# Kernel tuning notes

Hardware: AMD Instinct MI355X
Metric: run time of the kernel (lower is better)

## Reference

```python
import jax, jax.numpy as jnp
import numpy as np

H, N_EMB, D_EMB, D_UP = 1024, 8192, 512, 2048
B, T, BB, M, K_LABELS = 4, 4096, 512, 4096, 64


def _rms(x, w, eps=1e-6):
    xf = x.astype(jnp.float32)
    var = jnp.mean(xf * xf, axis=-1, keepdims=True)
    return (w * (xf * jax.lax.rsqrt(var + eps))).astype(x.dtype)


def setup_inputs() -> dict:
    key = jax.random.key(0)
    ks = jax.random.split(key, 8)
    bt = B * T
    inp = jax.random.normal(ks[0], (B, T, H), jnp.float32)
    w_k = jax.random.normal(ks[1], (N_EMB, H), jnp.float32) * 0.02
    w_v = jax.random.normal(ks[2], (N_EMB, D_EMB), jnp.float32) * 0.02
    w_up = jax.random.normal(ks[3], (D_UP, D_EMB), jnp.float32) * 0.02
    w_mix = jax.random.normal(ks[4], (H, D_UP + H), jnp.float32) * 0.02
    fw = jax.random.permutation(ks[5], bt)
    bw = jnp.argsort(fw)  # inverse permutation
    seq_sort = jax.random.randint(ks[6], (bt,), 0, K_LABELS)
    keep_cols = jnp.arange(M)  # keep first M of N_EMB rows
    emb_alloc = jnp.arange(N_EMB) % K_LABELS  # every label present among kept rows
    starts = jnp.zeros((bt,), jnp.int32)
    ends = jnp.full((bt,), M, jnp.int32)
    return {
        'input': inp, 'fw': fw, 'bw': bw, 'seq_sort': seq_sort,
        'keep_cols': keep_cols, 'emb_alloc': emb_alloc,
        'starts': starts, 'ends': ends, 'bb': BB,
        'w_k_weight': w_k, 'w_v_weight': w_v, 'w_up_weight': w_up,
        'w_mix_weight': w_mix,
        'norm_in_weight': jnp.ones((H,), jnp.float32),
        'norm_out_weight': jnp.ones((D_UP,), jnp.float32),
    }


def reference(input, fw, bw, seq_sort, keep_cols, emb_alloc, starts, ends, bb,
              w_k_weight, w_v_weight, w_up_weight, w_mix_weight,
              norm_in_weight, norm_out_weight):
    b, t, h = input.shape
    A = _rms(input, norm_in_weight)                      # [b,t,h]
    Bm = w_k_weight[keep_cols]                           # [m,h]
    Cm = w_v_weight[keep_cols]                           # [m,d_emb]
    la = emb_alloc[keep_cols]                            # [m]
    A = A.reshape(-1, h)[fw].reshape(-1, bb, h)          # [nb,bb,h]
    ss = seq_sort.reshape(-1, bb)                        # [nb,bb]
    st = starts.reshape(-1, bb).min(axis=-1)             # [nb]
    en = ends.reshape(-1, bb).max(axis=-1)               # [nb]
    # ragged per-block slice B[start:end] expressed as a kv range mask,
    # combined with the equality mask seq_sort[q] == emb_alloc[kv]
    scores = jnp.einsum('nqh,kh->nqk', A, Bm)            # [nb,bb,m]
    kv = jnp.arange(Bm.shape[0])
    mask = ((ss[:, :, None] == la[None, None, :])
            & (kv[None, None, :] >= st[:, None, None])
            & (kv[None, None, :] < en[:, None, None]))
    scores = jnp.where(mask, scores, -jnp.inf)
    p = jax.nn.softmax(scores, axis=-1)
    comb = jnp.einsum('nqk,kd->nqd', p, Cm)              # [nb,bb,d_emb]
    d_emb = Cm.shape[-1]
    comb = comb.reshape(-1, d_emb)[bw].reshape(b, t, d_emb)
    up = comb @ w_up_weight.T                            # [b,t,d_up]
    cat = jnp.concatenate([_rms(up, norm_out_weight), input], axis=-1)
    return cat @ w_mix_weight.T                          # [b,t,h]
```

## Files before the change

kernel.cpp:

```cpp
#include <hip/hip_runtime.h>
#include <hip/hip_bf16.h>
#include <cstdint>
#include <cstddef>

#define Hh 1024
#define D_EMB 512
#define D_UP 2048
#define BT 16384
#define BB_ 512
#define Mm 4096
#define NB 32
#define KL 64
#define NXCD 8
#define PMMAX 8192
#define QROWMAX 17408
#define MAXT 1088

typedef __attribute__((ext_vector_type(4))) float f4;
typedef __attribute__((ext_vector_type(4))) __bf16 bf4;
typedef __attribute__((ext_vector_type(8))) __bf16 bf8;
typedef __attribute__((ext_vector_type(4))) float f32x4;

__device__ __forceinline__ void gl_lds16(const void* g, void* l) {
  __builtin_amdgcn_global_load_lds((__attribute__((address_space(1))) void*)g,
                                   (__attribute__((address_space(3))) void*)l, 16, 0, 0);
}

__global__ __launch_bounds__(256) void k1_misc(const float* __restrict__ w_up,
                                               const float* __restrict__ w_mix,
                                               const float* __restrict__ w_nout,
                                               const int* __restrict__ keep,
                                               const int* __restrict__ emb,
                                               const int* __restrict__ starts,
                                               const int* __restrict__ ends,
                                               const int* __restrict__ seq_sort,
                                               __bf16* __restrict__ wupB,
                                               __bf16* __restrict__ wmixB,
                                               int* __restrict__ la,
                                               int* __restrict__ stA, int* __restrict__ enA,
                                               int* __restrict__ qidx,
                                               int* __restrict__ qoffA, int* __restrict__ qcntA,
                                               float* __restrict__ rowssq) {
  __shared__ int ssh[4], esh[4];
  __shared__ int cnt[KL], pos[KL], pref[KL];
  int b = blockIdx.x, tid = threadIdx.x;
  if (b < 1024) {
    int i = b * 256 + tid;
    f4 v = ((const f4*)w_up)[i];
    bf4 o = {(__bf16)v[0], (__bf16)v[1], (__bf16)v[2], (__bf16)v[3]};
    ((bf4*)wupB)[i] = o;
  } else if (b < 4096) {
    int i = (b - 1024) * 256 + tid;
    f4 v = ((const f4*)w_mix)[i];
    int kq = i % 768;
    if (kq < 512) {
      f4 wn = ((const f4*)w_nout)[kq];
      v[0] *= wn[0]; v[1] *= wn[1]; v[2] *= wn[2]; v[3] *= wn[3];
    }
    bf4 o = {(__bf16)v[0], (__bf16)v[1], (__bf16)v[2], (__bf16)v[3]};
    ((bf4*)wmixB)[i] = o;
  } else if (b < 4112) {
    int i = (b - 4096) * 256 + tid;
    if (i < Mm) la[i] = emb[keep[i]];
  } else if (b < 4144) {
    int n = b - 4112;
    int lane = tid & 63, wv = tid >> 6;
    int s1 = min(starts[n * BB_ + tid], starts[n * BB_ + tid + 256]);
    int e1 = max(ends[n * BB_ + tid], ends[n * BB_ + tid + 256]);
#pragma unroll
    for (int off = 32; off; off >>= 1) {
      s1 = min(s1, __shfl_xor(s1, off));
      e1 = max(e1, __shfl_xor(e1, off));
    }
    if (lane == 0) { ssh[wv] = s1; esh[wv] = e1; }
    __syncthreads();
    if (tid == 0) {
      int s = ssh[0], e = esh[0];
#pragma unroll
      for (int k = 1; k < 4; ++k) { s = min(s, ssh[k]); e = max(e, esh[k]); }
      stA[n] = s; enA[n] = e;
    }
  } else if (b < 4176) {
    int n = b - 4144;
    if (tid < KL) cnt[tid] = 0;
    __syncthreads();
    int s0 = seq_sort[n * BB_ + tid];
    int s1 = seq_sort[n * BB_ + tid + 256];
    atomicAdd(&cnt[s0], 1);
    atomicAdd(&cnt[s1], 1);
    __syncthreads();
    if (tid == 0) {
      int a = 0;
      for (int s = 0; s < KL; ++s) { pref[s] = a; a += cnt[s]; }
    }
    __syncthreads();
    if (tid < KL) {
      pos[tid] = pref[tid];
      qoffA[n * KL + tid] = pref[tid];
      qcntA[n * KL + tid] = cnt[tid];
    }
    __syncthreads();
    int p0 = atomicAdd(&pos[s0], 1);
    qidx[n * BB_ + p0] = n * BB_ + tid;
    int p1 = atomicAdd(&pos[s1], 1);
    qidx[n * BB_ + p1] = n * BB_ + tid + 256;
  } else {
    int i = (b - 4176) * 256 + tid;
    if (i < 4096) { f4 z = {0.f, 0.f, 0.f, 0.f}; ((f4*)rowssq)[i] = z; }
  }
}

__global__ __launch_bounds__(256) void k2_meta(const int* __restrict__ la,
                                               const int* __restrict__ qcntA,
                                               int* __restrict__ goff,
                                               int* __restrict__ boff, int* __restrict__ qtot,
                                               int* __restrict__ ptq, int* __restrict__ pb,
                                               int* __restrict__ taskS, int* __restrict__ taskT,
                                               int* __restrict__ ntt, int* __restrict__ pbTot) {
  __shared__ int cnt[KL];
  int tid = threadIdx.x;
  if (tid < KL) cnt[tid] = 0;
  __syncthreads();
  for (int k = tid; k < Mm; k += 256) atomicAdd(&cnt[la[k]], 1);
  if (tid < KL) {
    int s = tid, tot = 0;
    for (int n = 0; n < NB; ++n) { boff[n * KL + s] = tot; tot += qcntA[n * KL + s]; }
    qtot[s] = tot;
  }
  __syncthreads();
  if (tid == 0) {
    int a = 0;
    for (int s = 0; s < KL; ++s) { goff[s] = a; a += cnt[s]; }
    goff[KL] = a;
    int tb = 0, tk = 0, pk = 0;
    for (int s = 0; s < KL; ++s) {
      ptq[s] = tb;
      int nt = (qtot[s] + 15) >> 4;
      for (int t2 = 0; t2 < nt; ++t2) { taskS[tk] = s; taskT[tk] = t2; ++tk; }
      tb += nt;
      pb[s] = pk;
      int c2 = goff[s + 1] - goff[s];
      pk += (c2 + 63) & ~63;
    }
    ptq[KL] = tb;
    ntt[0] = tk;
    pbTot[0] = pk;
  }
}

__global__ __launch_bounds__(256) void place_kernel(const int* __restrict__ la,
                                                    const int* __restrict__ keep,
                                                    const int* __restrict__ goff,
                                                    int* __restrict__ gk,
                                                    int* __restrict__ ridx) {
  int s = blockIdx.x;
  int tid = threadIdx.x, lane = tid & 63, wv = tid >> 6;
  __shared__ int wc[4];
  __shared__ int run;
  if (tid == 0) run = goff[s];
  __syncthreads();
  for (int base = 0; base < Mm; base += 256) {
    int k = base + tid;
    bool f = (la[k] == s);
    unsigned long long msk = __ballot(f);
    int myidx = __popcll(msk & ((1ull << lane) - 1ull));
    if (lane == 0) wc[wv] = __popcll(msk);
    __syncthreads();
    int woff = 0, tot = 0;
#pragma unroll
    for (int w = 0; w < 4; ++w) {
      if (w < wv) woff += wc[w];
      tot += wc[w];
    }
    int rbase = run;
    if (f) {
      int p = rbase + woff + myidx;
      gk[p] = k;
      ridx[p] = keep[k];
    }
    __syncthreads();
    if (tid == 0) run = rbase + tot;
    __syncthreads();
  }
}

__global__ __launch_bounds__(256) void k4_idx(const int* __restrict__ goff,
                                              const int* __restrict__ pb,
                                              const int* __restrict__ ridx,
                                              int* __restrict__ pridx,
                                              const int* __restrict__ gk,
                                              const int* __restrict__ stA,
                                              const int* __restrict__ enA,
                                              int* __restrict__ loA, int* __restrict__ hiA,
                                              const int* __restrict__ qidx,
                                              const int* __restrict__ qoffA,
                                              const int* __restrict__ seq_sort,
                                              const int* __restrict__ boff,
                                              const int* __restrict__ ptq,
                                              int* __restrict__ qg2, int* __restrict__ gq,
                                              const int* __restrict__ qtot,
                                              __bf16* __restrict__ Qsw) {
  int b = blockIdx.x, tid = threadIdx.x;
  if (b < 64) {
    int s = b;
    int cnt2 = goff[s + 1] - goff[s];
    int padded = (cnt2 + 63) & ~63;
    int base = pb[s];
    for (int i = tid; i < padded; i += 256)
      pridx[base + i] = (i < cnt2) ? ridx[goff[s] + i] : -1;
  } else if (b < 72) {
    int i = (b - 64) * 256 + tid;
    if (i < NB * KL) {
      int n = i / KL, s = i % KL;
      int b0 = goff[s], e0 = goff[s + 1];
      int st = stA[n], en = enA[n];
      int lo = b0, hi = e0;
      while (lo < hi) { int mid = (lo + hi) >> 1; if (gk[mid] < st) lo = mid + 1; else hi = mid; }
      int L = lo;
      lo = b0; hi = e0;
      while (lo < hi) { int mid = (lo + hi) >> 1; if (gk[mid] < en) lo = mid + 1; else hi = mid; }
      loA[i] = pb[s] + (L - goff[s]);
      hiA[i] = pb[s] + (lo - goff[s]);
    }
  } else if (b < 136) {
    int e = (b - 72) * 256 + tid;
    int n = e >> 9;
    int q = qidx[e];
    int s = seq_sort[q];
    int i = (e & 511) - qoffA[n * KL + s];
    int gpos = ptq[s] * 16 + boff[n * KL + s] + i;
    qg2[gpos] = q;
    gq[q] = gpos;
  } else {
    int s = b - 136;
    int b0 = ptq[s] * 16 + qtot[s];
    int b1 = ptq[s + 1] * 16;
    bf8 z;
#pragma unroll
    for (int j = 0; j < 8; ++j) z[j] = (__bf16)0.f;
    for (int r = b0; r < b1; ++r)
      for (int e8 = tid; e8 < 128; e8 += 256)
        *(bf8*)&Qsw[(size_t)r * 1024 + e8 * 8] = z;
  }
}

__global__ __launch_bounds__(256) void k5_build(const float* __restrict__ wk,
                                                const float* __restrict__ wv_,
                                                const int* __restrict__ pridx,
                                                const int* __restrict__ pbTot,
                                                __bf16* __restrict__ Ksw,
                                                __bf16* __restrict__ Vsw) {
  __shared__ __align__(16) char shb[33792];
  int b = blockIdx.x, tid = threadIdx.x;
  if (b < 512) {
    int pt = b;
    if (pt * 16 >= pbTot[0]) return;
    auto Tk = (__bf16(*)[1040])shb;
    int rr = tid >> 4, lt = tid & 15;
    int src = pridx[pt * 16 + rr];
    for (int cc = 0; cc < 16; ++cc) {
      int i4 = cc * 16 + lt;
      f4 v = {0.f, 0.f, 0.f, 0.f};
      if (src >= 0) v = ((const f4*)(wk + (size_t)src * Hh))[i4];
      bf4 o = {(__bf16)v[0], (__bf16)v[1], (__bf16)v[2], (__bf16)v[3]};
      *(bf4*)&Tk[rr][i4 * 4] = o;
    }
    __syncthreads();
#pragma unroll
    for (int i = 0; i < 8; ++i) {
      int f = tid + 256 * i;
      int ks = f >> 6, ln = f & 63;
      int c2 = ln & 15, rg2 = ln >> 4;
      bf8 o = *(const bf8*)&Tk[c2][ks * 32 + rg2 * 8];
      *(bf8*)&Ksw[(size_t)pt * 16384 + (size_t)f * 8] = o;
    }
  } else {
    int pblk = b - 512;
    if (pblk * 32 >= pbTot[0]) return;
    auto Tv = (__bf16(*)[528])shb;
    int rr = tid >> 3, lt = tid & 7;
    int src = pridx[pblk * 32 + rr];
    for (int cc = 0; cc < 16; ++cc) {
      int i4 = cc * 8 + lt;
      f4 v = {0.f, 0.f, 0.f, 0.f};
      if (src >= 0) v = ((const f4*)(wv_ + (size_t)src * D_EMB))[i4];
      bf4 o = {(__bf16)v[0], (__bf16)v[1], (__bf16)v[2], (__bf16)v[3]};
      *(bf4*)&Tv[rr][i4 * 4] = o;
    }
    __syncthreads();
#pragma unroll
    for (int i = 0; i < 8; ++i) {
      int f = tid + 256 * i;
      int ff = f >> 6, ln = f & 63;
      int c2 = ln & 15, rg2 = ln >> 4;
      bf8 o;
#pragma unroll
      for (int j = 0; j < 8; ++j) o[j] = Tv[rg2 * 8 + j][ff * 16 + c2];
      *(bf8*)&Vsw[(size_t)pblk * 16384 + (size_t)f * 8] = o;
    }
  }
}

__global__ __launch_bounds__(256) void rms_in_kernel(const float* __restrict__ input,
                                                     const int* __restrict__ bw,
                                                     const int* __restrict__ gq,
                                                     const float* __restrict__ wn,
                                                     __bf16* __restrict__ Qsw,
                                                     __bf16* __restrict__ inb) {
  __shared__ __align__(16) __bf16 rowbuf[4][1024];
  int wv = threadIdx.x >> 6, lane = threadIdx.x & 63;
  int j = blockIdx.x * 4 + wv;
  const f4* src = (const f4*)(input + (size_t)j * Hh);
  f4 v[4];
  float ss = 0.f;
#pragma unroll
  for (int c = 0; c < 4; ++c) {
    v[c] = src[c * 64 + lane];
    ss += v[c][0] * v[c][0] + v[c][1] * v[c][1] + v[c][2] * v[c][2] + v[c][3] * v[c][3];
  }
#pragma unroll
  for (int off = 32; off; off >>= 1) ss += __shfl_xor(ss, off);
  float sc = rsqrtf(ss * (1.f / Hh) + 1e-6f);
  bf4* dstI = (bf4*)(inb + (size_t)j * Hh);
#pragma unroll
  for (int c = 0; c < 4; ++c) {
    bf4 o = {(__bf16)v[c][0], (__bf16)v[c][1], (__bf16)v[c][2], (__bf16)v[c][3]};
    dstI[c * 64 + lane] = o;
  }
  const f4* w4 = (const f4*)wn;
#pragma unroll
  for (int c = 0; c < 4; ++c) {
    f4 w = w4[c * 64 + lane];
    bf4 o = {(__bf16)(v[c][0] * sc * w[0]), (__bf16)(v[c][1] * sc * w[1]),
             (__bf16)(v[c][2] * sc * w[2]), (__bf16)(v[c][3] * sc * w[3])};
    *(bf4*)&rowbuf[wv][(c * 64 + lane) * 4] = o;
  }
  int gpos = gq[bw[j]];
  int qt2 = gpos >> 4, cq = gpos & 15;
#pragma unroll
  for (int h = 0; h < 2; ++h) {
    int k_ = lane + h * 64;
    int ks = k_ >> 2, rg2 = k_ & 3;
    bf8 o = *(const bf8*)&rowbuf[wv][ks * 32 + rg2 * 8];
    *(bf8*)(Qsw + (size_t)qt2 * 16384 + ks * 512 + (cq + 16 * rg2) * 8) = o;
  }
}

__global__ __launch_bounds__(256, 3) void attn7_kernel(const __bf16* __restrict__ Qsw,
                                                       const __bf16* __restrict__ Ksw,
                                                       const __bf16* __restrict__ Vsw,
                                                       const int* __restrict__ qg2,
                                                       const int* __restrict__ qtot,
                                                       const int* __restrict__ ptq,
                                                       const int* __restrict__ taskS,
                                                       const int* __restrict__ taskT,
                                                       const int* __restrict__ nttA,
                                                       const int* __restrict__ pb,
                                                       const int* __restrict__ loP,
                                                       const int* __restrict__ hiP,
                                                       const int* __restrict__ fw,
                                                       __bf16* __restrict__ comb) {
  __shared__ float Sb[16][66];
  __shared__ __align__(16) __bf16 Plds[16][72];
  __shared__ float scl_s[16], lrec[16];
  __shared__ __align__(16) __bf16 owb[16][528];
  int t = blockIdx.x;
  if (t >= nttA[0]) return;
  int tid = threadIdx.x, wv = tid >> 6, lane = tid & 63;
  int c = lane & 15, rg = lane >> 4;
  int s = taskS[t], tl = taskT[t];
  int qtp = ptq[s] + tl;
  int qcnt = min(16, qtot[s] - tl * 16);
  bool qv = c < qcnt;
  int q_l = qg2[qtp * 16 + (qv ? c : 0)];
  int n_l = q_l >> 9;
  int lo_l = qv ? loP[n_l * KL + s] : 0x7fffffff;
  int hi_l = qv ? hiP[n_l * KL + s] : 0;
  int tlo = lo_l, thi = hi_l;
#pragma unroll
  for (int off = 1; off < 64; off <<= 1) {
    tlo = min(tlo, __shfl_xor(tlo, off));
    thi = max(thi, __shfl_xor(thi, off));
  }
  if (tlo >= thi) return;
  int pbs = pb[s];
  const __bf16* Qb = Qsw + (size_t)qtp * 16384 + lane * 8;

  float m[4] = {-1e30f, -1e30f, -1e30f, -1e30f};
  float l[4] = {0.f, 0.f, 0.f, 0.f};
  f32x4 acc[8];
  f32x4 zero = {0.f, 0.f, 0.f, 0.f};
#pragma unroll
  for (int tt = 0; tt < 8; ++tt) acc[tt] = zero;

  int p0beg = pbs + ((tlo - pbs) & ~63);
  for (int p0 = p0beg; p0 < thi; p0 += 64) {
    const __bf16* Kb = Ksw + (size_t)((p0 >> 4) + wv) * 16384 + lane * 8;
    f32x4 sacc = zero;
#pragma unroll
    for (int ks = 0; ks < 32; ++ks) {
      bf8 qf = *(const bf8*)(Qb + ks * 512);
      bf8 kf = *(const bf8*)(Kb + ks * 512);
      sacc = __builtin_amdgcn_mfma_f32_16x16x32_bf16(kf, qf, sacc, 0, 0, 0);
    }
#pragma unroll
    for (int r = 0; r < 4; ++r) {
      int kv = p0 + wv * 16 + rg * 4 + r;
      Sb[c][wv * 16 + rg * 4 + r] = (kv >= lo_l && kv < hi_l) ? sacc[r] : -1e30f;
    }
    __syncthreads();

#pragma unroll
    for (int r = 0; r < 4; ++r) {
      int q = wv * 4 + r;
      float sv = Sb[q][lane];
      float cm = sv;
#pragma unroll
      for (int off = 32; off; off >>= 1) cm = fmaxf(cm, __shfl_xor(cm, off));
      float mn = fmaxf(m[r], cm);
      float sc2 = __expf(m[r] - mn);
      float pv = __expf(sv - mn);
      float ssum = pv;
#pragma unroll
      for (int off = 32; off; off >>= 1) ssum += __shfl_xor(ssum, off);
      l[r] = l[r] * sc2 + ssum;
      m[r] = mn;
      Plds[q][lane] = (__bf16)pv;
      if (lane == 0) scl_s[q] = sc2;
    }
    __syncthreads();

    float sf = scl_s[c];
#pragma unroll
    for (int tt = 0; tt < 8; ++tt) acc[tt] = acc[tt] * sf;
    bf8 pa0 = *(const bf8*)&Plds[c][rg * 8];
    bf8 pa1 = *(const bf8*)&Plds[c][32 + rg * 8];
    const __bf16* Vb = Vsw + (size_t)(p0 >> 5) * 16384 + lane * 8;
#pragma unroll
    for (int tt = 0; tt < 8; ++tt) {
      int ff = wv * 8 + tt;
      bf8 v0 = *(const bf8*)(Vb + ff * 512);
      bf8 v1 = *(const bf8*)(Vb + 16384 + ff * 512);
      acc[tt] = __builtin_amdgcn_mfma_f32_16x16x32_bf16(v0, pa0, acc[tt], 0, 0, 0);
      acc[tt] = __builtin_amdgcn_mfma_f32_16x16x32_bf16(v1, pa1, acc[tt], 0, 0, 0);
    }
    __syncthreads();
  }

  if (lane == 0) {
#pragma unroll
    for (int r = 0; r < 4; ++r) lrec[wv * 4 + r] = l[r];
  }
  __syncthreads();
  float inv = 1.f / lrec[c];
#pragma unroll
  for (int tt = 0; tt < 8; ++tt) {
    bf4 o;
#pragma unroll
    for (int r = 0; r < 4; ++r) o[r] = (__bf16)(acc[tt][r] * inv);
    *(bf4*)&owb[c][(wv * 8 + tt) * 16 + rg * 4] = o;
  }
  __syncthreads();
#pragma unroll
  for (int r4 = 0; r4 < 4; ++r4) {
    int q2 = wv * 4 + r4;
    if (q2 < qcnt) {
      size_t ob = (size_t)fw[qg2[qtp * 16 + q2]] * D_EMB;
      *(bf8*)(comb + ob + lane * 8) = *(const bf8*)&owb[q2][lane * 8];
    }
  }
}

template <bool OUT_BF16, bool SSQ, bool RS>
__global__ __launch_bounds__(512, 2) void gemm10(const __bf16* __restrict__ x0, int k0,
                                                 const __bf16* __restrict__ x1, int k1,
                                                 const __bf16* __restrict__ w,
                                                 void* __restrict__ outp, int Mt, int Nt,
                                                 float* __restrict__ rowssq, int rsTile) {
  __shared__ __align__(16) __bf16 lds[4][2][256 * 32];
  const int nwg = Mt * Nt;
  const int bid = blockIdx.x;
  const int swz = (bid % NXCD) * (nwg / NXCD) + bid / NXCD;
  const int m0 = (swz / Nt) * 256, n0 = (swz % Nt) * 256;
  const int K = k0 + k1;
  const int NT = K >> 5;
  const int N = Nt * 256;
  const int tid = threadIdx.x, lane = tid & 63, wvi = tid >> 6;
  const int wr = wvi >> 2, wc = wvi & 3;
  const int srow = tid >> 2;
  const int spb = (tid & 3) * 16;
  const int c = lane & 15, rg = lane >> 4;
  const int fa_off = c * 64 + ((rg ^ ((c >> 1) & 3)) << 4);
  const int r0 = (lane >> 4) * 4;

  auto stage = [&](int t) {
    int kg = t * 32;
    const __bf16* xs;
    int ld, kk;
    if (kg < k0) { xs = x0; ld = k0; kk = kg; }
    else         { xs = x1; ld = k1; kk = kg - k0; }
    int b = t & 3;
#pragma unroll
    for (int j = 0; j < 2; ++j) {
      int r = j * 128 + srow;
      int lcol = (spb ^ (((r >> 1) & 3) << 4)) >> 1;
      gl_lds16(xs + (size_t)(m0 + r) * ld + kk + lcol,
               (void*)((char*)&lds[b][0][0] + r * 64 + spb));
      gl_lds16(w + (size_t)(n0 + r) * K + kg + lcol,
               (void*)((char*)&lds[b][1][0] + r * 64 + spb));
    }
  };

  f32x4 acc[8][4];
  f32x4 zero = {0.f, 0.f, 0.f, 0.f};
#pragma unroll
  for (int a = 0; a < 8; ++a)
#pragma unroll
    for (int bnx = 0; bnx < 4; ++bnx) acc[a][bnx] = zero;

  auto compute = [&](int t) {
    const char* Ab = (const char*)&lds[t & 3][0][0];
    const char* Bb = (const char*)&lds[t & 3][1][0];
    bf8 afr[8], bfr[4];
#pragma unroll
    for (int fi = 0; fi < 8; ++fi)
      afr[fi] = *(const bf8*)(Ab + (wr * 128 + fi * 16) * 64 + fa_off);
#pragma unroll
    for (int ni = 0; ni < 4; ++ni)
      bfr[ni] = *(const bf8*)(Bb + (wc * 64 + ni * 16) * 64 + fa_off);
    __builtin_amdgcn_s_setprio(1);
#pragma unroll
    for (int fi = 0; fi < 8; ++fi)
#pragma unroll
      for (int ni = 0; ni < 4; ++ni)
        acc[fi][ni] = __builtin_amdgcn_mfma_f32_16x16x32_bf16(afr[fi], bfr[ni], acc[fi][ni], 0, 0, 0);
    __builtin_amdgcn_s_setprio(0);
  };

  auto apply_rs = [&]() {
#pragma unroll
    for (int mi = 0; mi < 8; ++mi) {
      int base = m0 + wr * 128 + mi * 16 + r0;
#pragma unroll
      for (int r = 0; r < 4; ++r) {
        float rsv = rsqrtf(rowssq[base + r] * (1.f / 2048.f) + 1e-6f);
#pragma unroll
        for (int ni = 0; ni < 4; ++ni) acc[mi][ni][r] *= rsv;
      }
    }
  };

  stage(0); stage(1); stage(2);
  asm volatile("s_waitcnt vmcnt(8)" ::: "memory");
  __builtin_amdgcn_s_barrier();

  for (int t = 0; t < NT - 3; ++t) {
    stage(t + 3);
    compute(t);
    if (RS) { if (t == rsTile) apply_rs(); }
    asm volatile("s_waitcnt vmcnt(8)" ::: "memory");
    __builtin_amdgcn_s_barrier();
  }
  compute(NT - 3);
  if (RS) { if (NT - 3 == rsTile) apply_rs(); }
  asm volatile("s_waitcnt vmcnt(4)" ::: "memory");
  __builtin_amdgcn_s_barrier();
  compute(NT - 2);
  if (RS) { if (NT - 2 == rsTile) apply_rs(); }
  asm volatile("s_waitcnt vmcnt(0)" ::: "memory");
  __builtin_amdgcn_s_barrier();
  compute(NT - 1);

  if (SSQ) {
#pragma unroll
    for (int mi = 0; mi < 8; ++mi) {
      float p[4];
#pragma unroll
      for (int r = 0; r < 4; ++r) {
        float a = 0.f;
#pragma unroll
        for (int ni = 0; ni < 4; ++ni) a += acc[mi][ni][r] * acc[mi][ni][r];
        p[r] = a;
      }
#pragma unroll
      for (int off = 1; off < 16; off <<= 1)
#pragma unroll
        for (int r = 0; r < 4; ++r) p[r] += __shfl_xor(p[r], off);
      if ((lane & 15) == 0) {
        int base = m0 + wr * 128 + mi * 16 + r0;
#pragma unroll
        for (int r = 0; r < 4; ++r) atomicAdd(&rowssq[base + r], p[r]);
      }
    }
  }

  const int cc = lane & 15;
#pragma unroll
  for (int mi = 0; mi < 8; ++mi) {
    int rowb = m0 + wr * 128 + mi * 16 + r0;
#pragma unroll
    for (int ni = 0; ni < 4; ++ni) {
      int col = n0 + wc * 64 + ni * 16 + cc;
#pragma unroll
      for (int r = 0; r < 4; ++r) {
        float v = acc[mi][ni][r];
        if (OUT_BF16)
          ((__bf16*)outp)[(size_t)(rowb + r) * N + col] = (__bf16)v;
        else
          ((float*)outp)[(size_t)(rowb + r) * N + col] = v;
      }
    }
  }
}

extern "C" void kernel_launch(void* const* d_in, const int* in_sizes, int n_in, void* d_out,
                              int out_size, void* d_ws, size_t ws_size, hipStream_t stream) {
  const float* input = (const float*)d_in[0];
  const int* fw = (const int*)d_in[1];
  const int* bw = (const int*)d_in[2];
  const int* seq_sort = (const int*)d_in[3];
  const int* keep_cols = (const int*)d_in[4];
  const int* emb_alloc = (const int*)d_in[5];
  const int* starts = (const int*)d_in[6];
  const int* ends = (const int*)d_in[7];
  const float* w_k = (const float*)d_in[9];
  const float* w_v = (const float*)d_in[10];
  const float* w_up = (const float*)d_in[11];
  const float* w_mix = (const float*)d_in[12];
  const float* w_nin = (const float*)d_in[13];
  const float* w_nout = (const float*)d_in[14];

  char* p = (char*)d_ws;
  auto take = [&](size_t b) {
    void* r = (void*)p;
    p += (b + 255) & ~(size_t)255;
    return r;
  };
  __bf16* inb = (__bf16*)take((size_t)BT * Hh * 2);
  __bf16* comb = (__bf16*)take((size_t)BT * D_EMB * 2);
  __bf16* wupB = (__bf16*)take((size_t)D_UP * D_EMB * 2);
  __bf16* wmixB = (__bf16*)take((size_t)Hh * (D_UP + Hh) * 2);
  float* rowssq = (float*)take((size_t)BT * 4);
  char* pB = p;
  __bf16* Ksw = (__bf16*)take((size_t)PMMAX * 1024 * 2);
  __bf16* Vsw = (__bf16*)take((size_t)PMMAX * 512 * 2);
  __bf16* Qsw = (__bf16*)take((size_t)QROWMAX * 1024 * 2);
  int* la = (int*)take(Mm * 4);
  int* stA = (int*)take(NB * 4);
  int* enA = (int*)take(NB * 4);
  int* goff = (int*)take((KL + 1) * 4);
  int* gk = (int*)take(Mm * 4);
  int* ridx = (int*)take(Mm * 4);
  int* pridx = (int*)take(PMMAX * 4);
  int* loA = (int*)take(NB * KL * 4);
  int* hiA = (int*)take(NB * KL * 4);
  int* qidx = (int*)take(BT * 4);
  int* qoffA = (int*)take(NB * KL * 4);
  int* qcntA = (int*)take(NB * KL * 4);
  int* boff = (int*)take(NB * KL * 4);
  int* qtot = (int*)take(KL * 4);
  int* ptq = (int*)take((KL + 1) * 4);
  int* pb = (int*)take(KL * 4);
  int* taskS = (int*)take(MAXT * 4);
  int* taskT = (int*)take(MAXT * 4);
  int* ntt = (int*)take(4);
  int* pbTot = (int*)take(4);
  int* qg2 = (int*)take(QROWMAX * 4);
  int* gq = (int*)take(BT * 4);
  __bf16* up = (__bf16*)pB;

  k1_misc<<<4192, 256, 0, stream>>>(w_up, w_mix, w_nout, keep_cols, emb_alloc, starts, ends,
                                    seq_sort, wupB, wmixB, la, stA, enA, qidx, qoffA, qcntA,
                                    rowssq);
  k2_meta<<<1, 256, 0, stream>>>(la, qcntA, goff, boff, qtot, ptq, pb, taskS, taskT, ntt, pbTot);
  place_kernel<<<KL, 256, 0, stream>>>(la, keep_cols, goff, gk, ridx);
  k4_idx<<<200, 256, 0, stream>>>(goff, pb, ridx, pridx, gk, stA, enA, loA, hiA, qidx, qoffA,
                                  seq_sort, boff, ptq, qg2, gq, qtot, Qsw);
  k5_build<<<768, 256, 0, stream>>>(w_k, w_v, pridx, pbTot, Ksw, Vsw);
  rms_in_kernel<<<BT / 4, 256, 0, stream>>>(input, bw, gq, w_nin, Qsw, inb);
  attn7_kernel<<<MAXT, 256, 0, stream>>>(Qsw, Ksw, Vsw, qg2, qtot, ptq, taskS, taskT, ntt, pb,
                                         loA, hiA, fw, comb);
  gemm10<true, true, false><<<BT / 256 * (D_UP / 256), 512, 0, stream>>>(
      comb, D_EMB, (const __bf16*)nullptr, 0, wupB, (void*)up, BT / 256, D_UP / 256, rowssq, -1);
  gemm10<false, false, true><<<BT / 256 * (Hh / 256), 512, 0, stream>>>(
      up, D_UP, inb, Hh, wmixB, d_out, BT / 256, Hh / 256, rowssq, 63);
}
```

Before: 342.4 us.

## Restructure GEMM main loop into 64-wide K tiles with interleaved quarter-tile staging

```diff
diff --git a/kernel.cpp b/kernel.cpp
--- a/kernel.cpp
+++ b/kernel.cpp
@@ -472,18 +472,18 @@
 }
 
 template <bool OUT_BF16, bool SSQ, bool RS>
-__global__ __launch_bounds__(512, 2) void gemm10(const __bf16* __restrict__ x0, int k0,
+__global__ __launch_bounds__(512, 2) void gemm11(const __bf16* __restrict__ x0, int k0,
                                                  const __bf16* __restrict__ x1, int k1,
                                                  const __bf16* __restrict__ w,
                                                  void* __restrict__ outp, int Mt, int Nt,
                                                  float* __restrict__ rowssq, int rsTile) {
-  __shared__ __align__(16) __bf16 lds[4][2][256 * 32];
+  __shared__ __align__(16) __bf16 lds[2][2][2][256 * 32];
   const int nwg = Mt * Nt;
   const int bid = blockIdx.x;
   const int swz = (bid % NXCD) * (nwg / NXCD) + bid / NXCD;
   const int m0 = (swz / Nt) * 256, n0 = (swz % Nt) * 256;
   const int K = k0 + k1;
-  const int NT = K >> 5;
+  const int NT = K >> 6;
   const int N = Nt * 256;
   const int tid = threadIdx.x, lane = tid & 63, wvi = tid >> 6;
   const int wr = wvi >> 2, wc = wvi & 3;
@@ -493,21 +493,21 @@
   const int fa_off = c * 64 + ((rg ^ ((c >> 1) & 3)) << 4);
   const int r0 = (lane >> 4) * 4;
 
-  auto stage = [&](int t) {
-    int kg = t * 32;
+  auto stage_region = [&](int t, int ab, int ch) {
+    int kg = t * 64 + ch * 32;
     const __bf16* xs;
     int ld, kk;
-    if (kg < k0) { xs = x0; ld = k0; kk = kg; }
-    else         { xs = x1; ld = k1; kk = kg - k0; }
-    int b = t & 3;
+    if (ab == 0) {
+      if (kg < k0) { xs = x0; ld = k0; kk = kg; }
+      else         { xs = x1; ld = k1; kk = kg - k0; }
+    } else { xs = w; ld = K; kk = kg; }
+    int rowbase = (ab == 0) ? m0 : n0;
+    char* base = (char*)&lds[t & 1][ab][ch][0];
 #pragma unroll
     for (int j = 0; j < 2; ++j) {
       int r = j * 128 + srow;
       int lcol = (spb ^ (((r >> 1) & 3) << 4)) >> 1;
-      gl_lds16(xs + (size_t)(m0 + r) * ld + kk + lcol,
-               (void*)((char*)&lds[b][0][0] + r * 64 + spb));
-      gl_lds16(w + (size_t)(n0 + r) * K + kg + lcol,
-               (void*)((char*)&lds[b][1][0] + r * 64 + spb));
+      gl_lds16(xs + (size_t)(rowbase + r) * ld + kk + lcol, (void*)(base + r * 64 + spb));
     }
   };
 
@@ -518,25 +518,6 @@
 #pragma unroll
     for (int bnx = 0; bnx < 4; ++bnx) acc[a][bnx] = zero;
 
-  auto compute = [&](int t) {
-    const char* Ab = (const char*)&lds[t & 3][0][0];
-    const char* Bb = (const char*)&lds[t & 3][1][0];
-    bf8 afr[8], bfr[4];
-#pragma unroll
-    for (int fi = 0; fi < 8; ++fi)
-      afr[fi] = *(const bf8*)(Ab + (wr * 128 + fi * 16) * 64 + fa_off);
-#pragma unroll
-    for (int ni = 0; ni < 4; ++ni)
-      bfr[ni] = *(const bf8*)(Bb + (wc * 64 + ni * 16) * 64 + fa_off);
-    __builtin_amdgcn_s_setprio(1);
-#pragma unroll
-    for (int fi = 0; fi < 8; ++fi)
-#pragma unroll
-      for (int ni = 0; ni < 4; ++ni)
-        acc[fi][ni] = __builtin_amdgcn_mfma_f32_16x16x32_bf16(afr[fi], bfr[ni], acc[fi][ni], 0, 0, 0);
-    __builtin_amdgcn_s_setprio(0);
-  };
-
   auto apply_rs = [&]() {
 #pragma unroll
     for (int mi = 0; mi < 8; ++mi) {
@@ -550,26 +531,97 @@
     }
   };
 
-  stage(0); stage(1); stage(2);
-  asm volatile("s_waitcnt vmcnt(8)" ::: "memory");
+  stage_region(0, 0, 0);
+  stage_region(0, 1, 0);
+  stage_region(0, 0, 1);
+  stage_region(0, 1, 1);
+  stage_region(1, 0, 0);
+  stage_region(1, 1, 0);
   __builtin_amdgcn_s_barrier();
 
-  for (int t = 0; t < NT - 3; ++t) {
-    stage(t + 3);
-    compute(t);
+  for (int t = 0; t < NT; ++t) {
+    const int bsel = t & 1;
+    bf8 afr[8], bfr[2];
+    if (t < NT - 1) asm volatile("s_waitcnt vmcnt(8)" ::: "memory");
+    else            asm volatile("s_waitcnt vmcnt(4)" ::: "memory");
+    {
+      const char* Ab = (const char*)&lds[bsel][0][0][0];
+      const char* Bb = (const char*)&lds[bsel][1][0][0];
+#pragma unroll
+      for (int fi = 0; fi < 8; ++fi)
+        afr[fi] = *(const bf8*)(Ab + (wr * 128 + fi * 16) * 64 + fa_off);
+#pragma unroll
+      for (int j = 0; j < 2; ++j)
+        bfr[j] = *(const bf8*)(Bb + (wc * 64 + j * 16) * 64 + fa_off);
+    }
+    if (t + 1 < NT) stage_region(t + 1, 0, 1);
+    __builtin_amdgcn_s_barrier();
+    __builtin_amdgcn_s_setprio(1);
+#pragma unroll
+    for (int fi = 0; fi < 8; ++fi)
+#pragma unroll
+      for (int j = 0; j < 2; ++j)
+        acc[fi][j] = __builtin_amdgcn_mfma_f32_16x16x32_bf16(afr[fi], bfr[j], acc[fi][j], 0, 0, 0);
+    __builtin_amdgcn_s_setprio(0);
+    __builtin_amdgcn_s_barrier();
+    {
+      const char* Bb = (const char*)&lds[bsel][1][0][0];
+#pragma unroll
+      for (int j = 0; j < 2; ++j)
+        bfr[j] = *(const bf8*)(Bb + (wc * 64 + (2 + j) * 16) * 64 + fa_off);
+    }
+    if (t + 1 < NT) stage_region(t + 1, 1, 1);
+    __builtin_amdgcn_s_barrier();
+    __builtin_amdgcn_s_setprio(1);
+#pragma unroll
+    for (int fi = 0; fi < 8; ++fi)
+#pragma unroll
+      for (int j = 0; j < 2; ++j)
+        acc[fi][2 + j] =
+            __builtin_amdgcn_mfma_f32_16x16x32_bf16(afr[fi], bfr[j], acc[fi][2 + j], 0, 0, 0);
+    __builtin_amdgcn_s_setprio(0);
+    __builtin_amdgcn_s_barrier();
+    if (t < NT - 1) asm volatile("s_waitcnt vmcnt(8)" ::: "memory");
+    else            asm volatile("s_waitcnt vmcnt(0)" ::: "memory");
+    {
+      const char* Ab = (const char*)&lds[bsel][0][1][0];
+      const char* Bb = (const char*)&lds[bsel][1][1][0];
+#pragma unroll
+      for (int fi = 0; fi < 8; ++fi)
+        afr[fi] = *(const bf8*)(Ab + (wr * 128 + fi * 16) * 64 + fa_off);
+#pragma unroll
+      for (int j = 0; j < 2; ++j)
+        bfr[j] = *(const bf8*)(Bb + (wc * 64 + j * 16) * 64 + fa_off);
+    }
+    if (t + 2 < NT) stage_region(t + 2, 0, 0);
+    __builtin_amdgcn_s_barrier();
+    __builtin_amdgcn_s_setprio(1);
+#pragma unroll
+    for (int fi = 0; fi < 8; ++fi)
+#pragma unroll
+      for (int j = 0; j < 2; ++j)
+        acc[fi][j] = __builtin_amdgcn_mfma_f32_16x16x32_bf16(afr[fi], bfr[j], acc[fi][j], 0, 0, 0);
+    __builtin_amdgcn_s_setprio(0);
+    __builtin_amdgcn_s_barrier();
+    {
+      const char* Bb = (const char*)&lds[bsel][1][1][0];
+#pragma unroll
+      for (int j = 0; j < 2; ++j)
+        bfr[j] = *(const bf8*)(Bb + (wc * 64 + (2 + j) * 16) * 64 + fa_off);
+    }
+    if (t + 2 < NT) stage_region(t + 2, 1, 0);
+    __builtin_amdgcn_s_barrier();
+    __builtin_amdgcn_s_setprio(1);
+#pragma unroll
+    for (int fi = 0; fi < 8; ++fi)
+#pragma unroll
+      for (int j = 0; j < 2; ++j)
+        acc[fi][2 + j] =
+            __builtin_amdgcn_mfma_f32_16x16x32_bf16(afr[fi], bfr[j], acc[fi][2 + j], 0, 0, 0);
+    __builtin_amdgcn_s_setprio(0);
     if (RS) { if (t == rsTile) apply_rs(); }
-    asm volatile("s_waitcnt vmcnt(8)" ::: "memory");
     __builtin_amdgcn_s_barrier();
   }
-  compute(NT - 3);
-  if (RS) { if (NT - 3 == rsTile) apply_rs(); }
-  asm volatile("s_waitcnt vmcnt(4)" ::: "memory");
-  __builtin_amdgcn_s_barrier();
-  compute(NT - 2);
-  if (RS) { if (NT - 2 == rsTile) apply_rs(); }
-  asm volatile("s_waitcnt vmcnt(0)" ::: "memory");
-  __builtin_amdgcn_s_barrier();
-  compute(NT - 1);
 
   if (SSQ) {
 #pragma unroll
@@ -680,8 +732,8 @@
   rms_in_kernel<<<BT / 4, 256, 0, stream>>>(input, bw, gq, w_nin, Qsw, inb);
   attn7_kernel<<<MAXT, 256, 0, stream>>>(Qsw, Ksw, Vsw, qg2, qtot, ptq, taskS, taskT, ntt, pb,
                                          loA, hiA, fw, comb);
-  gemm10<true, true, false><<<BT / 256 * (D_UP / 256), 512, 0, stream>>>(
+  gemm11<true, true, false><<<BT / 256 * (D_UP / 256), 512, 0, stream>>>(
       comb, D_EMB, (const __bf16*)nullptr, 0, wupB, (void*)up, BT / 256, D_UP / 256, rowssq, -1);
-  gemm10<false, false, true><<<BT / 256 * (Hh / 256), 512, 0, stream>>>(
-      up, D_UP, inb, Hh, wmixB, d_out, BT / 256, Hh / 256, rowssq, 63);
-}
+  gemm11<false, false, true><<<BT / 256 * (Hh / 256), 512, 0, stream>>>(
+      up, D_UP, inb, Hh, wmixB, d_out, BT / 256, Hh / 256, rowssq, 31);
+}
```

After: 347.4 us. Within noise of the previous version (+1.5%).

## Pre-swizzle GEMM weights into MFMA fragment order and load B directly to registers

Applied to the files above, without the earlier changes.

```diff
diff --git a/kernel.cpp b/kernel.cpp
--- a/kernel.cpp
+++ b/kernel.cpp
@@ -34,8 +34,8 @@
                                                const int* __restrict__ starts,
                                                const int* __restrict__ ends,
                                                const int* __restrict__ seq_sort,
-                                               __bf16* __restrict__ wupB,
-                                               __bf16* __restrict__ wmixB,
+                                               __bf16* __restrict__ wupF,
+                                               __bf16* __restrict__ wmixF,
                                                int* __restrict__ la,
                                                int* __restrict__ stA, int* __restrict__ enA,
                                                int* __restrict__ qidx,
@@ -45,20 +45,23 @@
   __shared__ int cnt[KL], pos[KL], pref[KL];
   int b = blockIdx.x, tid = threadIdx.x;
   if (b < 1024) {
-    int i = b * 256 + tid;
-    f4 v = ((const f4*)w_up)[i];
+    int i4 = b * 256 + tid;
+    f4 v = ((const f4*)w_up)[i4];
+    int n = i4 >> 7, k4 = i4 & 127;
+    int nt = n >> 4, c = n & 15, ks = k4 >> 3, rg = (k4 >> 1) & 3, ii = (k4 & 1) * 4;
     bf4 o = {(__bf16)v[0], (__bf16)v[1], (__bf16)v[2], (__bf16)v[3]};
-    ((bf4*)wupB)[i] = o;
+    *(bf4*)&wupF[((((nt << 4) + ks) << 6) + rg * 16 + c) * 8 + ii] = o;
   } else if (b < 4096) {
-    int i = (b - 1024) * 256 + tid;
-    f4 v = ((const f4*)w_mix)[i];
-    int kq = i % 768;
-    if (kq < 512) {
-      f4 wn = ((const f4*)w_nout)[kq];
+    int i4 = (b - 1024) * 256 + tid;
+    f4 v = ((const f4*)w_mix)[i4];
+    int n = i4 / 768, k4 = i4 % 768;
+    if (k4 < 512) {
+      f4 wn = ((const f4*)w_nout)[k4];
       v[0] *= wn[0]; v[1] *= wn[1]; v[2] *= wn[2]; v[3] *= wn[3];
     }
+    int nt = n >> 4, c = n & 15, ks = k4 >> 3, rg = (k4 >> 1) & 3, ii = (k4 & 1) * 4;
     bf4 o = {(__bf16)v[0], (__bf16)v[1], (__bf16)v[2], (__bf16)v[3]};
-    ((bf4*)wmixB)[i] = o;
+    *(bf4*)&wmixF[((nt * 96 + ks) * 64 + rg * 16 + c) * 8 + ii] = o;
   } else if (b < 4112) {
     int i = (b - 4096) * 256 + tid;
     if (i < Mm) la[i] = emb[keep[i]];
@@ -472,16 +475,16 @@
 }
 
 template <bool OUT_BF16, bool SSQ, bool RS>
-__global__ __launch_bounds__(512, 2) void gemm10(const __bf16* __restrict__ x0, int k0,
+__global__ __launch_bounds__(512, 2) void gemm12(const __bf16* __restrict__ x0, int k0,
                                                  const __bf16* __restrict__ x1, int k1,
-                                                 const __bf16* __restrict__ w,
+                                                 const __bf16* __restrict__ Bf,
                                                  void* __restrict__ outp, int Mt, int Nt,
                                                  float* __restrict__ rowssq, int rsTile) {
-  __shared__ __align__(16) __bf16 lds[4][2][256 * 32];
+  __shared__ __align__(16) __bf16 lds[4][256 * 32];
   const int nwg = Mt * Nt;
   const int bid = blockIdx.x;
   const int swz = (bid % NXCD) * (nwg / NXCD) + bid / NXCD;
-  const int m0 = (swz / Nt) * 256, n0 = (swz % Nt) * 256;
+  const int m0 = (swz % Mt) * 256, n0 = (swz / Mt) * 256;
   const int K = k0 + k1;
   const int NT = K >> 5;
   const int N = Nt * 256;
@@ -492,23 +495,27 @@
   const int c = lane & 15, rg = lane >> 4;
   const int fa_off = c * 64 + ((rg ^ ((c >> 1) & 3)) << 4);
   const int r0 = (lane >> 4) * 4;
-
-  auto stage = [&](int t) {
+  const int ntb = (n0 >> 4) + wc * 4;
+
+  auto stageA = [&](int t) {
     int kg = t * 32;
     const __bf16* xs;
     int ld, kk;
     if (kg < k0) { xs = x0; ld = k0; kk = kg; }
     else         { xs = x1; ld = k1; kk = kg - k0; }
-    int b = t & 3;
+    char* base = (char*)&lds[t & 3][0];
 #pragma unroll
     for (int j = 0; j < 2; ++j) {
       int r = j * 128 + srow;
       int lcol = (spb ^ (((r >> 1) & 3) << 4)) >> 1;
-      gl_lds16(xs + (size_t)(m0 + r) * ld + kk + lcol,
-               (void*)((char*)&lds[b][0][0] + r * 64 + spb));
-      gl_lds16(w + (size_t)(n0 + r) * K + kg + lcol,
-               (void*)((char*)&lds[b][1][0] + r * 64 + spb));
-    }
+      gl_lds16(xs + (size_t)(m0 + r) * ld + kk + lcol, (void*)(base + r * 64 + spb));
+    }
+  };
+
+  auto bload = [&](int t, bf8* bfr) {
+#pragma unroll
+    for (int ni = 0; ni < 4; ++ni)
+      bfr[ni] = *(const bf8*)(Bf + (((size_t)(ntb + ni) * NT + t) << 9) + lane * 8);
   };
 
   f32x4 acc[8][4];
@@ -518,25 +525,6 @@
 #pragma unroll
     for (int bnx = 0; bnx < 4; ++bnx) acc[a][bnx] = zero;
 
-  auto compute = [&](int t) {
-    const char* Ab = (const char*)&lds[t & 3][0][0];
-    const char* Bb = (const char*)&lds[t & 3][1][0];
-    bf8 afr[8], bfr[4];
-#pragma unroll
-    for (int fi = 0; fi < 8; ++fi)
-      afr[fi] = *(const bf8*)(Ab + (wr * 128 + fi * 16) * 64 + fa_off);
-#pragma unroll
-    for (int ni = 0; ni < 4; ++ni)
-      bfr[ni] = *(const bf8*)(Bb + (wc * 64 + ni * 16) * 64 + fa_off);
-    __builtin_amdgcn_s_setprio(1);
-#pragma unroll
-    for (int fi = 0; fi < 8; ++fi)
-#pragma unroll
-      for (int ni = 0; ni < 4; ++ni)
-        acc[fi][ni] = __builtin_amdgcn_mfma_f32_16x16x32_bf16(afr[fi], bfr[ni], acc[fi][ni], 0, 0, 0);
-    __builtin_amdgcn_s_setprio(0);
-  };
-
   auto apply_rs = [&]() {
 #pragma unroll
     for (int mi = 0; mi < 8; ++mi) {
@@ -550,26 +538,36 @@
     }
   };
 
-  stage(0); stage(1); stage(2);
+  bf8 bcur[4], bnext[4];
+  stageA(0); stageA(1); stageA(2);
+  bload(0, bcur);
   asm volatile("s_waitcnt vmcnt(8)" ::: "memory");
   __builtin_amdgcn_s_barrier();
 
-  for (int t = 0; t < NT - 3; ++t) {
-    stage(t + 3);
-    compute(t);
+  for (int t = 0; t < NT; ++t) {
+    if (t + 1 < NT) bload(t + 1, bnext);
+    if (t + 3 < NT) stageA(t + 3);
+    {
+      const char* Ab = (const char*)&lds[t & 3][0];
+      bf8 afr[8];
+#pragma unroll
+      for (int fi = 0; fi < 8; ++fi)
+        afr[fi] = *(const bf8*)(Ab + (wr * 128 + fi * 16) * 64 + fa_off);
+      __builtin_amdgcn_s_setprio(1);
+#pragma unroll
+      for (int fi = 0; fi < 8; ++fi)
+#pragma unroll
+        for (int ni = 0; ni < 4; ++ni)
+          acc[fi][ni] = __builtin_amdgcn_mfma_f32_16x16x32_bf16(afr[fi], bcur[ni], acc[fi][ni], 0, 0, 0);
+      __builtin_amdgcn_s_setprio(0);
+    }
     if (RS) { if (t == rsTile) apply_rs(); }
-    asm volatile("s_waitcnt vmcnt(8)" ::: "memory");
+    if (t < NT - 3) asm volatile("s_waitcnt vmcnt(12)" ::: "memory");
+    else            asm volatile("s_waitcnt vmcnt(0)" ::: "memory");
     __builtin_amdgcn_s_barrier();
-  }
-  compute(NT - 3);
-  if (RS) { if (NT - 3 == rsTile) apply_rs(); }
-  asm volatile("s_waitcnt vmcnt(4)" ::: "memory");
-  __builtin_amdgcn_s_barrier();
-  compute(NT - 2);
-  if (RS) { if (NT - 2 == rsTile) apply_rs(); }
-  asm volatile("s_waitcnt vmcnt(0)" ::: "memory");
-  __builtin_amdgcn_s_barrier();
-  compute(NT - 1);
+#pragma unroll
+    for (int ni = 0; ni < 4; ++ni) bcur[ni] = bnext[ni];
+  }
 
   if (SSQ) {
 #pragma unroll
@@ -638,8 +636,8 @@
   };
   __bf16* inb = (__bf16*)take((size_t)BT * Hh * 2);
   __bf16* comb = (__bf16*)take((size_t)BT * D_EMB * 2);
-  __bf16* wupB = (__bf16*)take((size_t)D_UP * D_EMB * 2);
-  __bf16* wmixB = (__bf16*)take((size_t)Hh * (D_UP + Hh) * 2);
+  __bf16* wupF = (__bf16*)take((size_t)D_UP * D_EMB * 2);
+  __bf16* wmixF = (__bf16*)take((size_t)Hh * (D_UP + Hh) * 2);
   float* rowssq = (float*)take((size_t)BT * 4);
   char* pB = p;
   __bf16* Ksw = (__bf16*)take((size_t)PMMAX * 1024 * 2);
@@ -670,7 +668,7 @@
   __bf16* up = (__bf16*)pB;
 
   k1_misc<<<4192, 256, 0, stream>>>(w_up, w_mix, w_nout, keep_cols, emb_alloc, starts, ends,
-                                    seq_sort, wupB, wmixB, la, stA, enA, qidx, qoffA, qcntA,
+                                    seq_sort, wupF, wmixF, la, stA, enA, qidx, qoffA, qcntA,
                                     rowssq);
   k2_meta<<<1, 256, 0, stream>>>(la, qcntA, goff, boff, qtot, ptq, pb, taskS, taskT, ntt, pbTot);
   place_kernel<<<KL, 256, 0, stream>>>(la, keep_cols, goff, gk, ridx);
@@ -680,8 +678,8 @@
   rms_in_kernel<<<BT / 4, 256, 0, stream>>>(input, bw, gq, w_nin, Qsw, inb);
   attn7_kernel<<<MAXT, 256, 0, stream>>>(Qsw, Ksw, Vsw, qg2, qtot, ptq, taskS, taskT, ntt, pb,
                                          loA, hiA, fw, comb);
-  gemm10<true, true, false><<<BT / 256 * (D_UP / 256), 512, 0, stream>>>(
-      comb, D_EMB, (const __bf16*)nullptr, 0, wupB, (void*)up, BT / 256, D_UP / 256, rowssq, -1);
-  gemm10<false, false, true><<<BT / 256 * (Hh / 256), 512, 0, stream>>>(
-      up, D_UP, inb, Hh, wmixB, d_out, BT / 256, Hh / 256, rowssq, 63);
-}
+  gemm12<true, true, false><<<BT / 256 * (D_UP / 256), 512, 0, stream>>>(
+      comb, D_EMB, (const __bf16*)nullptr, 0, wupF, (void*)up, BT / 256, D_UP / 256, rowssq, -1);
+  gemm12<false, false, true><<<BT / 256 * (Hh / 256), 512, 0, stream>>>(
+      up, D_UP, inb, Hh, wmixF, d_out, BT / 256, Hh / 256, rowssq, 63);
+}
```

Measured after the change: 412.3 us. +20.4%, slower.
